# Optimization experiments

Hardware: AMD Instinct MI355X
Metric: run time of the kernel (lower is better)

The kernel has to match this reference:

```python
import jax, jax.numpy as jnp
import numpy as np
from jax import lax

B, T, L, HID = 128, 8, 8, 64  # batch, horizon(=num_layers), lstm layers, hidden

def setup_inputs() -> dict:
    key = jax.random.key(0)
    ks = jax.random.split(key, 40)
    def rn(i, shape, s=0.02):
        return jax.random.normal(ks[i], shape, dtype=jnp.float32) * s
    inp = {
        'image_data': jax.random.normal(ks[0], (B, 3, 192, 256), jnp.float32),
        'action_input_data': jax.random.normal(ks[1], (B, T, 2), jnp.float32),
        'ground_truth_data': jax.random.normal(ks[2], (B, T, 6), jnp.float32),
        'conv1_w': rn(3, (32, 3, 5, 5)), 'conv1_b': rn(4, (32,)),
        'conv2_w': rn(5, (64, 32, 3, 3)), 'conv2_b': rn(6, (64,)),
        'conv3_w': rn(7, (64, 64, 3, 3)), 'conv3_b': rn(8, (64,)),
        'fc1_w': rn(9, (256, 42240)), 'fc1_b': rn(10, (256,)),
        'fc2_w': rn(11, (128, 256)), 'fc2_b': rn(12, (128,)),
        'lowd1_w': rn(13, (128, 128)), 'lowd1_b': rn(14, (128,)),
        'lowd2_w': rn(15, (128, 128)), 'lowd2_b': rn(16, (128,)),
        'act1_w': rn(17, (16, 2)), 'act1_b': rn(18, (16,)),
        'act2_w': rn(19, (16, 16)), 'act2_b': rn(20, (16,)),
        'lstm_Wih0': rn(21, (4 * HID, 16)),
        'lstm_Wih': rn(22, (L - 1, 4 * HID, HID)),
        'lstm_Whh': rn(23, (L, 4 * HID, HID)),
        'lstm_bih': rn(24, (L, 4 * HID)),
        'lstm_bhh': rn(25, (L, 4 * HID)),
        'out1_w': rn(26, (32, 64)), 'out1_b': rn(27, (32,)),
        'out2_w': rn(28, (4, 32)), 'out2_b': rn(29, (4,)),
        'BATCH_SIZE': B, 'horizon': T,
    }
    return inp

def _lin(x, w, b):
    return x @ w.T + b

def _conv(x, w, b):
    y = lax.conv_general_dilated(x, w, (2, 2), 'VALID',
                                 dimension_numbers=('NCHW', 'OIHW', 'NCHW'))
    return y + b[None, :, None, None]

def _lstm(x, h0, c0, Wih0, Wih, Whh, bih, bhh):
    # x: (B,T,16); h0/c0: (L,B,HID). PyTorch gate order: i,f,g,o.
    inp = x
    for l in range(L):
        Wih_l = Wih0 if l == 0 else Wih[l - 1]
        bih_l, bhh_l, Whh_l = bih[l], bhh[l], Whh[l]
        def step(carry, xt):
            h, c = carry
            g = xt @ Wih_l.T + bih_l + h @ Whh_l.T + bhh_l
            i_, f_, g_, o_ = jnp.split(g, 4, axis=-1)
            c = jax.nn.sigmoid(f_) * c + jax.nn.sigmoid(i_) * jnp.tanh(g_)
            h = jax.nn.sigmoid(o_) * jnp.tanh(c)
            return (h, c), h
        _, ys = lax.scan(step, (h0[l], c0[l]), jnp.swapaxes(inp, 0, 1))
        inp = jnp.swapaxes(ys, 0, 1)  # (B,T,HID)
    return inp

def reference(image_data, action_input_data, ground_truth_data,
              conv1_w, conv1_b, conv2_w, conv2_b, conv3_w, conv3_b,
              fc1_w, fc1_b, fc2_w, fc2_b,
              lowd1_w, lowd1_b, lowd2_w, lowd2_b,
              act1_w, act1_b, act2_w, act2_b,
              lstm_Wih0, lstm_Wih, lstm_Whh, lstm_bih, lstm_bhh,
              out1_w, out1_b, out2_w, out2_b,
              BATCH_SIZE, horizon):
    # CNN image pipeline
    x = jax.nn.relu(_conv(image_data, conv1_w, conv1_b))
    x = jax.nn.relu(_conv(x, conv2_w, conv2_b))
    x = _conv(x, conv3_w, conv3_b)
    x = x.reshape(x.shape[0], -1)  # (B, 42240)
    x = jax.nn.relu(_lin(x, fc1_w, fc1_b))
    cnn_out1 = _lin(x, fc2_w, fc2_b)  # (B,128)
    cnn_out2 = _lin(jax.nn.relu(_lin(cnn_out1, lowd1_w, lowd1_b)), lowd2_w, lowd2_b)
    # action pipeline
    a = _lin(jax.nn.relu(_lin(action_input_data, act1_w, act1_b)), act2_w, act2_b)
    # split: first 64 -> c0, second 64 -> h0; broadcast over layers
    c_tmp, h_tmp = cnn_out2[:, :HID], cnn_out2[:, HID:]
    h0 = jnp.broadcast_to(h_tmp[None], (L, h_tmp.shape[0], HID))
    c0 = jnp.broadcast_to(c_tmp[None], (L, c_tmp.shape[0], HID))
    lstm_out = _lstm(a, h0, c0, lstm_Wih0, lstm_Wih, lstm_Whh, lstm_bih, lstm_bhh)
    mo = _lin(jax.nn.relu(_lin(lstm_out, out1_w, out1_b)), out2_w, out2_b)  # (B,T,4)
    # batched yaw rotation (vectorizes the original per-sample loop)
    yaw = ground_truth_data[:, 0, 5]
    cy, sy = jnp.cos(yaw), jnp.sin(yaw)
    z, o = jnp.zeros_like(cy), jnp.ones_like(cy)
    rot = jnp.stack([cy, -sy, z, sy, cy, z, z, z, o], axis=-1).reshape(-1, 3, 3)
    pos = jnp.einsum('bti,bij->btj', mo[:, :, :3], rot) + ground_truth_data[:, 0, 1:4][:, None, :]
    return jnp.concatenate([pos, mo[:, :, 3:4]], axis=-1)
```

## Files before the change

kernel.cpp:

```cpp
#include <hip/hip_runtime.h>
#include <cstdint>

#define DEV __device__ __forceinline__

typedef __attribute__((ext_vector_type(8))) short bf16x8;
typedef __attribute__((ext_vector_type(4))) float f32x4;
typedef __attribute__((ext_vector_type(2))) __fp16 h2t;
typedef __attribute__((ext_vector_type(4))) unsigned int u32x4;
typedef unsigned long long u64;

DEV unsigned short f2bf(float f) {
    unsigned u = __float_as_uint(f);
    unsigned r = u + 0x7fffu + ((u >> 16) & 1u);
    return (unsigned short)(r >> 16);
}
DEV uint32_t pkbf2(float a, float b) {
    return (uint32_t)f2bf(a) | ((uint32_t)f2bf(b) << 16);
}
DEV uint32_t pkh2(float a, float b) {
    h2t p = __builtin_amdgcn_cvt_pkrtz(a, b);
    union { h2t h; uint32_t u; } c;
    c.h = p;
    return c.u;
}
DEV float dot2(uint32_t w, uint32_t x, float acc) {
    union { uint32_t u; h2t h; } a, b;
    a.u = w; b.u = x;
    return __builtin_amdgcn_fdot2(a.h, b.h, acc, false);
}
DEV float sigm(float x) { return __builtin_amdgcn_rcpf(1.f + __expf(-x)); }
DEV float tanh_(float x) { return fmaf(2.f, sigm(2.f * x), -1.f); }
DEV uint32_t packpair(float h) {
    float hs = __int_as_float(__builtin_amdgcn_ds_swizzle(__float_as_int(h), 0x041F));
    return pkh2(h, hs);
}
DEV uint32_t comp4v(u32x4 v, int e) {
    return (e == 0) ? v[0] : (e == 1) ? v[1] : (e == 2) ? v[2] : v[3];
}
DEV u64 pack4bf(float a, float b, float c, float d) {
    unsigned lo = (unsigned)f2bf(a) | ((unsigned)f2bf(b) << 16);
    unsigned hi = (unsigned)f2bf(c) | ((unsigned)f2bf(d) << 16);
    return (u64)lo | ((u64)hi << 32);
}

__global__ __launch_bounds__(256) void k_wprep(const float* __restrict__ w1,
                                               const float* __restrict__ w2,
                                               const float* __restrict__ w3,
                                               unsigned short* __restrict__ w1t,
                                               unsigned short* __restrict__ w2t,
                                               unsigned short* __restrict__ w3t) {
    int i = blockIdx.x * 256 + threadIdx.x;
    if (i < 32 * 128) {
        int oc = i >> 7, k = i & 127;
        int cc = k >> 3, u = (k >> 2) & 1, c = k & 3;
        int r = cc / 3, kx = 2 * (cc - 3 * r) + u;
        w1t[i] = (cc < 15 && kx < 5 && c < 3) ? f2bf(w1[oc * 75 + c * 25 + r * 5 + kx])
                                              : (unsigned short)0;
    } else if (i < 32 * 128 + 64 * 288) {
        int j = i - 32 * 128;
        int oc = j / 288, k = j - oc * 288;
        int pos = k >> 5, c = k & 31;
        int ocr = ((c >> 2) & 1) * 16 + (c >> 3) * 4 + (c & 3);
        w2t[j] = f2bf(w2[oc * 288 + ocr * 9 + pos]);
    } else if (i < 32 * 128 + 64 * 288 + 64 * 576) {
        int j = i - 32 * 128 - 64 * 288;
        int oc = j / 576, k = j - oc * 576;
        int pos = k >> 6, c = k & 63;
        w3t[j] = f2bf(w3[oc * 576 + c * 9 + pos]);
    }
}

__global__ __launch_bounds__(256) void k_wprep_lstm(const float* __restrict__ Wih0,
                                                    const float* __restrict__ Wih,
                                                    const float* __restrict__ Whh,
                                                    uint32_t* __restrict__ wpk) {
    int idx = blockIdx.x * 256 + threadIdx.x;
    int lane = idx & 63;
    int j = (idx >> 6) & 63;
    int l = idx >> 12;
    int g = j >> 4, q = j & 15;
    int r = g * 64 + lane;
    uint32_t ov[4];
#pragma unroll
    for (int e = 0; e < 4; ++e) {
        int p = q * 4 + e;
        float w0, w1;
        if (p < 32) {
            int k0 = 2 * p;
            if (l == 0) {
                w0 = (k0 < 16) ? Wih0[r * 16 + k0] : 0.f;
                w1 = (k0 + 1 < 16) ? Wih0[r * 16 + k0 + 1] : 0.f;
            } else {
                const float* base = Wih + ((size_t)(l - 1) * 256 + r) * 64;
                w0 = base[k0];
                w1 = base[k0 + 1];
            }
        } else {
            int k0 = 2 * (p - 32);
            const float* base = Whh + ((size_t)l * 256 + r) * 64;
            w0 = base[k0];
            w1 = base[k0 + 1];
        }
        ov[e] = pkh2(w0, w1);
    }
    uint4 v;
    v.x = ov[0]; v.y = ov[1]; v.z = ov[2]; v.w = ov[3];
    ((uint4*)wpk)[idx] = v;
}

__global__ __launch_bounds__(256, 3) void k_conv1m(const float* __restrict__ img,
                                                   const unsigned short* __restrict__ w1t,
                                                   const float* __restrict__ bias,
                                                   unsigned short* __restrict__ out) {
    int b = blockIdx.x, y0 = blockIdx.y * 4;
    int tid = threadIdx.x;
    __shared__ __align__(16) unsigned short lds[12 * 1040];
    char* lb = (char*)lds;
    const float* ib = img + (size_t)b * 3 * 192 * 256;
    float t0[11], t1[11], t2[11];
#pragma unroll
    for (int r = 0; r < 11; ++r) {
        int row = 2 * y0 + r;
        if (row > 191) row = 191;
        const float* ip = ib + row * 256 + tid;
        t0[r] = ip[0];
        t1[r] = ip[192 * 256];
        t2[r] = ip[2 * 192 * 256];
    }
    __builtin_amdgcn_sched_barrier(0);
#pragma unroll
    for (int r = 0; r < 11; ++r) {
        uint32_t lo = (uint32_t)f2bf(t0[r]) | ((uint32_t)f2bf(t1[r]) << 16);
        *(u64*)(lb + r * 2080 + tid * 8) = (u64)lo | ((u64)f2bf(t2[r]) << 32);
    }
    *(u64*)(lb + 11 * 2080 + tid * 8) = 0ull;
    __syncthreads();
    int wave = tid >> 6, lane = tid & 63;
    int quad = lane >> 4, nl = lane & 15;
    int ly = wave;
    float4 bv0 = *(const float4*)(bias + quad * 4);
    float4 bv1 = *(const float4*)(bias + 16 + quad * 4);
    f32x4 acc[8][2];
#pragma unroll
    for (int nt = 0; nt < 8; ++nt) {
        acc[nt][0][0] = bv0.x; acc[nt][0][1] = bv0.y; acc[nt][0][2] = bv0.z; acc[nt][0][3] = bv0.w;
        acc[nt][1][0] = bv1.x; acc[nt][1][1] = bv1.y; acc[nt][1][2] = bv1.z; acc[nt][1][3] = bv1.w;
    }
#pragma unroll
    for (int ks = 0; ks < 4; ++ks) {
        int cc = ks * 4 + quad;
        int r = cc / 3, kxp = cc - 3 * r;
        int rb = (2 * ly + r) * 2080 + kxp * 16 + nl * 16;
        bf16x8 af0 = *(const bf16x8*)(w1t + (nl) * 128 + ks * 32 + quad * 8);
        bf16x8 af1 = *(const bf16x8*)(w1t + (16 + nl) * 128 + ks * 32 + quad * 8);
#pragma unroll
        for (int nt = 0; nt < 8; ++nt) {
            bf16x8 bv = *(const bf16x8*)(lb + rb + nt * 256);
            acc[nt][0] = __builtin_amdgcn_mfma_f32_16x16x32_bf16(af0, bv, acc[nt][0], 0, 0, 0);
            acc[nt][1] = __builtin_amdgcn_mfma_f32_16x16x32_bf16(af1, bv, acc[nt][1], 0, 0, 0);
        }
    }
    int y = y0 + ly;
    if (y < 94) {
#pragma unroll
        for (int nt = 0; nt < 8; ++nt) {
            int x = nt * 16 + nl;
            if (x < 126) {
                f32x4 a0 = acc[nt][0], a1 = acc[nt][1];
                u64 lo = pack4bf(fmaxf(a0[0], 0.f), fmaxf(a0[1], 0.f),
                                 fmaxf(a0[2], 0.f), fmaxf(a0[3], 0.f));
                u64 hi = pack4bf(fmaxf(a1[0], 0.f), fmaxf(a1[1], 0.f),
                                 fmaxf(a1[2], 0.f), fmaxf(a1[3], 0.f));
                uint4 st;
                st.x = (uint32_t)lo; st.y = (uint32_t)(lo >> 32);
                st.z = (uint32_t)hi; st.w = (uint32_t)(hi >> 32);
                *(uint4*)(out + (((size_t)b * 94 + y) * 126 + x) * 32 + quad * 8) = st;
            }
        }
    }
}

__global__ __launch_bounds__(256, 1) void k_conv2m(const unsigned short* __restrict__ in,
                                                   const unsigned short* __restrict__ w2t,
                                                   const float* __restrict__ bias,
                                                   unsigned short* __restrict__ out) {
    int b = blockIdx.x, xh = blockIdx.y, yh = blockIdx.z;
    int tid = threadIdx.x;
    int wave = tid >> 6, lane = tid & 63;
    int quad = lane >> 4, nl = lane & 15;
    int mtg = wave & 1, ntg = wave >> 1;
    __shared__ __align__(16) char lds[4 * 4680];
    const u64* in64 = (const u64*)in;

    bf16x8 wfa[9], wfb[9];
#pragma unroll
    for (int ks = 0; ks < 9; ++ks) {
        wfa[ks] = *(const bf16x8*)(w2t + ((mtg * 2 + 0) * 16 + nl) * 288 + ks * 32 + quad * 8);
        wfb[ks] = *(const bf16x8*)(w2t + ((mtg * 2 + 1) * 16 + nl) * 288 + ks * 32 + quad * 8);
    }
    float4 bv0 = *(const float4*)(bias + (mtg * 2 + 0) * 16 + quad * 4);
    float4 bv1 = *(const float4*)(bias + (mtg * 2 + 1) * 16 + quad * 4);

    int y0 = yh * 23;
    int rr = tid >> 7, li = tid & 127;

    {
        int y2 = 2 * y0 + rr;
        const u64* s = in64 + ((size_t)(b * 94 + y2) * 126 + 62 * xh) * 8;
        int slot = y2 & 3;
        u64 g0[4];
#pragma unroll
        for (int j = 0; j < 4; ++j) { int idx = li + j * 128; g0[j] = (idx < 504) ? s[idx] : 0ull; }
#pragma unroll
        for (int j = 0; j < 4; ++j) {
            int idx = li + j * 128;
            if (idx < 504) *(u64*)(lds + slot * 4680 + (idx >> 3) * 72 + (idx & 7) * 8) = g0[j];
        }
        int y2b = 2 * y0 + 2;
        const u64* s2 = in64 + ((size_t)(b * 94 + y2b) * 126 + 62 * xh) * 8;
        int slot2 = y2b & 3;
        u64 g1[2];
#pragma unroll
        for (int j = 0; j < 2; ++j) { int idx = tid + j * 256; g1[j] = (idx < 504) ? s2[idx] : 0ull; }
#pragma unroll
        for (int j = 0; j < 2; ++j) {
            int idx = tid + j * 256;
            if (idx < 504) *(u64*)(lds + slot2 * 4680 + (idx >> 3) * 72 + (idx & 7) * 8) = g1[j];
        }
    }
    u64 g[4];
    {
        int y2 = 2 * y0 + 3 + rr;
        const u64* s = in64 + ((size_t)(b * 94 + y2) * 126 + 62 * xh) * 8;
#pragma unroll
        for (int j = 0; j < 4; ++j) { int idx = li + j * 128; g[j] = (idx < 504) ? s[idx] : 0ull; }
    }
    __syncthreads();

    int xl = ntg * 16 + nl;
    for (int yy = 0; yy < 23; ++yy) {
        int y = y0 + yy;
        f32x4 acc0, acc1;
        acc0[0] = bv0.x; acc0[1] = bv0.y; acc0[2] = bv0.z; acc0[3] = bv0.w;
        acc1[0] = bv1.x; acc1[1] = bv1.y; acc1[2] = bv1.z; acc1[3] = bv1.w;
        int sb0 = ((2 * y) & 3) * 4680;
        int sb1 = ((2 * y + 1) & 3) * 4680;
        int sb2 = ((2 * y + 2) & 3) * 4680;
#pragma unroll
        for (int ks = 0; ks < 9; ++ks) {
            const int r = ks / 3, kx = ks - r * 3;
            int sb = (r == 0) ? sb0 : (r == 1) ? sb1 : sb2;
            union { u64 d[2]; bf16x8 v; } bb;
            const char* base = lds + sb + (2 * xl + kx) * 72 + quad * 16;
            bb.d[0] = *(const u64*)(base);
            bb.d[1] = *(const u64*)(base + 8);
            acc0 = __builtin_amdgcn_mfma_f32_16x16x32_bf16(wfa[ks], bb.v, acc0, 0, 0, 0);
            acc1 = __builtin_amdgcn_mfma_f32_16x16x32_bf16(wfb[ks], bb.v, acc1, 0, 0, 0);
        }
        if (xl < 31) {
            int xg = xh * 31 + xl;
            u64 p0 = pack4bf(fmaxf(acc0[0], 0.f), fmaxf(acc0[1], 0.f),
                             fmaxf(acc0[2], 0.f), fmaxf(acc0[3], 0.f));
            u64 p1 = pack4bf(fmaxf(acc1[0], 0.f), fmaxf(acc1[1], 0.f),
                             fmaxf(acc1[2], 0.f), fmaxf(acc1[3], 0.f));
            *(u64*)(out + (((size_t)b * 46 + y) * 62 + xg) * 64 + (mtg * 2 + 0) * 16 + quad * 4) = p0;
            *(u64*)(out + (((size_t)b * 46 + y) * 62 + xg) * 64 + (mtg * 2 + 1) * 16 + quad * 4) = p1;
        }
        __syncthreads();
        {
            int row = 2 * y + 3 + rr;
            int slot = row & 3;
#pragma unroll
            for (int j = 0; j < 4; ++j) {
                int idx = li + j * 128;
                if (idx < 504) *(u64*)(lds + slot * 4680 + (idx >> 3) * 72 + (idx & 7) * 8) = g[j];
            }
        }
        if (yy < 22) {
            int y2 = 2 * y + 5 + rr;
            if (y2 > 93) y2 = 93;
            const u64* s = in64 + ((size_t)(b * 94 + y2) * 126 + 62 * xh) * 8;
#pragma unroll
            for (int j = 0; j < 4; ++j) { int idx = li + j * 128; g[j] = (idx < 504) ? s[idx] : 0ull; }
        }
        __syncthreads();
    }
}

__global__ __launch_bounds__(256, 1) void k_conv3m(const unsigned short* __restrict__ in,
                                                   const unsigned short* __restrict__ w3t,
                                                   const float* __restrict__ bias,
                                                   unsigned short* __restrict__ out) {
    int b = blockIdx.x, xh = blockIdx.y, yh = blockIdx.z;
    int tid = threadIdx.x;
    int wave = tid >> 6, lane = tid & 63;
    int quad = lane >> 4, nl = lane & 15;
    __shared__ __align__(16) char lds[4 * 4488];
    const u64* in64 = (const u64*)in;

    bf16x8 wf[18];
#pragma unroll
    for (int ks = 0; ks < 18; ++ks)
        wf[ks] = *(const bf16x8*)(w3t + (wave * 16 + nl) * 576 + ks * 32 + quad * 8);
    float4 bv = *(const float4*)(bias + wave * 16 + quad * 4);

    int y0 = yh * 11;
    int rr = tid >> 7, li = tid & 127;

    {
        int y2 = 2 * y0 + rr;
        const u64* s = in64 + ((size_t)(b * 46 + y2) * 62 + 30 * xh) * 16;
        int slot = y2 & 3;
        u64 g0[4];
#pragma unroll
        for (int j = 0; j < 4; ++j) { int idx = li + j * 128; g0[j] = (idx < 496) ? s[idx] : 0ull; }
#pragma unroll
        for (int j = 0; j < 4; ++j) {
            int idx = li + j * 128;
            if (idx < 496) *(u64*)(lds + slot * 4488 + (idx >> 4) * 136 + (idx & 15) * 8) = g0[j];
        }
        int y2b = 2 * y0 + 2;
        const u64* s2 = in64 + ((size_t)(b * 46 + y2b) * 62 + 30 * xh) * 16;
        int slot2 = y2b & 3;
        u64 g1[2];
#pragma unroll
        for (int j = 0; j < 2; ++j) { int idx = tid + j * 256; g1[j] = (idx < 496) ? s2[idx] : 0ull; }
#pragma unroll
        for (int j = 0; j < 2; ++j) {
            int idx = tid + j * 256;
            if (idx < 496) *(u64*)(lds + slot2 * 4488 + (idx >> 4) * 136 + (idx & 15) * 8) = g1[j];
        }
    }
    u64 g[4];
    {
        int y2 = 2 * y0 + 3 + rr;
        const u64* s = in64 + ((size_t)(b * 46 + y2) * 62 + 30 * xh) * 16;
#pragma unroll
        for (int j = 0; j < 4; ++j) { int idx = li + j * 128; g[j] = (idx < 496) ? s[idx] : 0ull; }
    }
    __syncthreads();

    for (int yy = 0; yy < 11; ++yy) {
        int y = y0 + yy;
        f32x4 acc;
        acc[0] = bv.x; acc[1] = bv.y; acc[2] = bv.z; acc[3] = bv.w;
        int sb0 = ((2 * y) & 3) * 4488;
        int sb1 = ((2 * y + 1) & 3) * 4488;
        int sb2 = ((2 * y + 2) & 3) * 4488;
#pragma unroll
        for (int ks = 0; ks < 18; ++ks) {
            const int pos = ks >> 1, half = ks & 1;
            const int r = pos / 3, kx = pos - r * 3;
            int sb = (r == 0) ? sb0 : (r == 1) ? sb1 : sb2;
            union { u64 d[2]; bf16x8 v; } bb;
            const char* base = lds + sb + (2 * nl + kx) * 136 + half * 64 + quad * 16;
            bb.d[0] = *(const u64*)(base);
            bb.d[1] = *(const u64*)(base + 8);
            acc = __builtin_amdgcn_mfma_f32_16x16x32_bf16(wf[ks], bb.v, acc, 0, 0, 0);
        }
        if (nl < 15) {
            int xg = xh * 15 + nl;
#pragma unroll
            for (int r2 = 0; r2 < 4; ++r2)
                out[(size_t)b * 42240 + (wave * 16 + quad * 4 + r2) * 660 + y * 30 + xg] = f2bf(acc[r2]);
        }
        __syncthreads();
        {
            int row = 2 * y + 3 + rr;
            int slot = row & 3;
#pragma unroll
            for (int j = 0; j < 4; ++j) {
                int idx = li + j * 128;
                if (idx < 496) *(u64*)(lds + slot * 4488 + (idx >> 4) * 136 + (idx & 15) * 8) = g[j];
            }
        }
        if (yy < 10) {
            int y2 = 2 * y + 5 + rr;
            if (y2 > 45) y2 = 45;
            const u64* s = in64 + ((size_t)(b * 46 + y2) * 62 + 30 * xh) * 16;
#pragma unroll
            for (int j = 0; j < 4; ++j) { int idx = li + j * 128; g[j] = (idx < 496) ? s[idx] : 0ull; }
        }
        __syncthreads();
    }
}

__global__ __launch_bounds__(256) void k_fc1_mfma(const unsigned short* __restrict__ A,
                                                  const float* __restrict__ W,
                                                  float* __restrict__ part) {
    int kc = blockIdx.x;
    int nb = blockIdx.y;
    int tid = threadIdx.x;
    int wave = tid >> 6, lane = tid & 63;
    int m16 = lane & 15, quad = lane >> 4;
    __shared__ __align__(16) char lw[2][64 * 80];
    __shared__ __align__(16) char la[2][128 * 80];
    int k0 = kc * 704;
    int wrow = tid >> 2, wseg = tid & 3;
    const float* wsrc = W + (size_t)(nb * 64 + wrow) * 42240 + k0 + wseg * 8;
    int arow = tid >> 1, aseg = tid & 1;
    const uint4* asrc = (const uint4*)(A + (size_t)arow * 42240 + k0) + aseg * 2;
    float4 wr0 = ((const float4*)wsrc)[0];
    float4 wr1 = ((const float4*)wsrc)[1];
    uint4 ar0 = asrc[0];
    uint4 ar1 = asrc[1];
    f32x4 acc[8] = {};
    for (int ks = 0; ks < 22; ++ks) {
        int buf = ks & 1;
        uint4 wp;
        wp.x = pkbf2(wr0.x, wr0.y); wp.y = pkbf2(wr0.z, wr0.w);
        wp.z = pkbf2(wr1.x, wr1.y); wp.w = pkbf2(wr1.z, wr1.w);
        *(uint4*)(lw[buf] + wrow * 80 + wseg * 16) = wp;
        *(uint4*)(la[buf] + arow * 80 + aseg * 32) = ar0;
        *(uint4*)(la[buf] + arow * 80 + aseg * 32 + 16) = ar1;
        if (ks < 21) {
            wsrc += 32;
            asrc += 4;
            wr0 = ((const float4*)wsrc)[0];
            wr1 = ((const float4*)wsrc)[1];
            ar0 = asrc[0];
            ar1 = asrc[1];
        }
        __syncthreads();
        bf16x8 wf = *(const bf16x8*)(lw[buf] + (wave * 16 + m16) * 80 + quad * 16);
        const char* lab = la[buf] + m16 * 80 + quad * 16;
#pragma unroll
        for (int tm = 0; tm < 8; ++tm) {
            bf16x8 af = *(const bf16x8*)(lab + tm * 16 * 80);
            acc[tm] = __builtin_amdgcn_mfma_f32_16x16x32_bf16(af, wf, acc[tm], 0, 0, 0);
        }
    }
    int n = nb * 64 + wave * 16 + m16;
    float* pb = part + ((size_t)kc * 128) * 256 + n;
#pragma unroll
    for (int tm = 0; tm < 8; ++tm) {
        int row = tm * 16 + quad * 4;
#pragma unroll
        for (int r = 0; r < 4; ++r) pb[(size_t)(row + r) * 256] = acc[tm][r];
    }
}

__global__ __launch_bounds__(256) void k_head(const float* __restrict__ part,
                                              const float* __restrict__ f1b,
                                              const float* __restrict__ w2, const float* __restrict__ b2,
                                              const float* __restrict__ lw1, const float* __restrict__ lb1,
                                              const float* __restrict__ lw2, const float* __restrict__ lb2,
                                              float* __restrict__ cnn2) {
    int b = blockIdx.x, t = threadIdx.x;
    __shared__ float xa[256];
    __shared__ float xb[128];
    __shared__ float xc[128];
    __shared__ float pp[256];
    float s = f1b[t];
#pragma unroll
    for (int kc = 0; kc < 60; ++kc) s += part[((size_t)kc * 128 + b) * 256 + t];
    xa[t] = fmaxf(s, 0.f);
    __syncthreads();
    int n = t & 127, half = t >> 7;
    float acc = half ? 0.f : b2[n];
    {
        const float* w2r = w2 + n * 256 + half * 128;
        const float* xar = xa + half * 128;
#pragma unroll
        for (int k = 0; k < 128; ++k) acc = fmaf(xar[k], w2r[k], acc);
    }
    pp[t] = acc;
    __syncthreads();
    if (t < 128) xb[t] = pp[t] + pp[t + 128];
    __syncthreads();
    acc = half ? 0.f : lb1[n];
    {
        const float* l1r = lw1 + n * 128 + half * 64;
        const float* xbr = xb + half * 64;
#pragma unroll
        for (int k = 0; k < 64; ++k) acc = fmaf(xbr[k], l1r[k], acc);
    }
    pp[t] = acc;
    __syncthreads();
    if (t < 128) xc[t] = fmaxf(pp[t] + pp[t + 128], 0.f);
    __syncthreads();
    acc = half ? 0.f : lb2[n];
    {
        const float* l2r = lw2 + n * 128 + half * 64;
        const float* xcr = xc + half * 64;
#pragma unroll
        for (int k = 0; k < 64; ++k) acc = fmaf(xcr[k], l2r[k], acc);
    }
    pp[t] = acc;
    __syncthreads();
    if (t < 128) cnn2[b * 128 + t] = pp[t] + pp[t + 128];
}

__global__ __launch_bounds__(256) void k_act(const float* __restrict__ ain,
                                             const float* __restrict__ w1, const float* __restrict__ b1,
                                             const float* __restrict__ w2, const float* __restrict__ b2,
                                             float* __restrict__ abuf) {
    int idx = blockIdx.x * 256 + threadIdx.x;
    float x0 = ain[idx * 2], x1 = ain[idx * 2 + 1];
    float h1[16];
#pragma unroll
    for (int i = 0; i < 16; ++i)
        h1[i] = fmaxf(fmaf(x0, w1[i * 2], fmaf(x1, w1[i * 2 + 1], b1[i])), 0.f);
#pragma unroll
    for (int i = 0; i < 16; ++i) {
        float a = b2[i];
#pragma unroll
        for (int j = 0; j < 16; ++j) a = fmaf(h1[j], w2[i * 16 + j], a);
        abuf[idx * 16 + i] = a;
    }
}

__global__ __launch_bounds__(512, 2) void k_lstm(const float* __restrict__ abuf,
                                                 const float* __restrict__ cnn2,
                                                 const uint32_t* __restrict__ wpk,
                                                 const float* __restrict__ bih,
                                                 const float* __restrict__ bhh,
                                                 float* __restrict__ lout) {
    int b = blockIdx.x;
    int tid = threadIdx.x;
    int w = tid >> 6, lane = tid & 63;
    int sl = w >> 1, pt = w & 1;
    __shared__ uint32_t hbuf[2][3][32];
    __shared__ uint32_t h3pk[8][32];
    __shared__ float4 pex[8][64];

    uint32_t xq[8];
#pragma unroll
    for (int t = 0; t < 8; ++t) {
        float x0 = 0.f, x1 = 0.f;
        if (lane < 8) {
            const float* ap = abuf + (b * 8 + t) * 16 + 2 * lane;
            x0 = ap[0];
            x1 = ap[1];
        }
        xq[t] = pkh2(x0, x1);
    }
    float h0 = cnn2[b * 128 + 64 + lane];
    float c0 = cnn2[b * 128 + lane];
    const u32x4* wbase = (const u32x4*)wpk;

#pragma unroll
    for (int P = 0; P < 2; ++P) {
        const int L = P * 4 + sl;
        u32x4 wreg[4][8];
#pragma unroll
        for (int g = 0; g < 4; ++g)
#pragma unroll
            for (int q = 0; q < 8; ++q)
                wreg[g][q] = wbase[(size_t)L * 4096 + (g * 16 + pt * 8 + q) * 64 + lane];
        float bias0 = 0.f, bias1 = 0.f, bias2 = 0.f, bias3 = 0.f;
        if (pt == 0) {
            bias0 = bih[L * 256 + lane] + bhh[L * 256 + lane];
            bias1 = bih[L * 256 + 64 + lane] + bhh[L * 256 + 64 + lane];
            bias2 = bih[L * 256 + 128 + lane] + bhh[L * 256 + 128 + lane];
            bias3 = bih[L * 256 + 192 + lane] + bhh[L * 256 + 192 + lane];
        }
        float h = h0, c = c0;
        uint32_t hpk = packpair(h0);

        for (int s = 0; s < 11; ++s) {
            bool act = (s >= sl && s < sl + 8);
            float a0 = bias0, a1 = bias1, a2 = bias2, a3 = bias3;
            if (act) {
                if (pt == 0) {
                    uint32_t xcur;
                    if (sl == 0)
                        xcur = (P == 0) ? xq[0] : h3pk[s][lane & 31];
                    else
                        xcur = hbuf[(s & 1) ^ 1][sl - 1][lane & 31];
#pragma unroll
                    for (int m = 0; m < 32; ++m) {
                        uint32_t bx = (uint32_t)__builtin_amdgcn_readlane((int)xcur, m);
                        int q = m >> 2, e = m & 3;
                        a0 = dot2(comp4v(wreg[0][q], e), bx, a0);
                        a1 = dot2(comp4v(wreg[1][q], e), bx, a1);
                        a2 = dot2(comp4v(wreg[2][q], e), bx, a2);
                        a3 = dot2(comp4v(wreg[3][q], e), bx, a3);
                    }
                } else {
#pragma unroll
                    for (int m = 0; m < 32; ++m) {
                        uint32_t bh2 = (uint32_t)__builtin_amdgcn_readlane((int)hpk, 2 * m);
                        int q = m >> 2, e = m & 3;
                        a0 = dot2(comp4v(wreg[0][q], e), bh2, a0);
                        a1 = dot2(comp4v(wreg[1][q], e), bh2, a1);
                        a2 = dot2(comp4v(wreg[2][q], e), bh2, a2);
                        a3 = dot2(comp4v(wreg[3][q], e), bh2, a3);
                    }
                }
                float4 pv;
                pv.x = a0; pv.y = a1; pv.z = a2; pv.w = a3;
                pex[w][lane] = pv;
            }
            __syncthreads();
            if (act) {
                float4 po = pex[w ^ 1][lane];
                float g0 = a0 + po.x, g1 = a1 + po.y, g2 = a2 + po.z, g3 = a3 + po.w;
                float gi = sigm(g0), gf = sigm(g1), gv = tanh_(g2), go = sigm(g3);
                c = gf * c + gi * gv;
                h = go * tanh_(c);
                hpk = packpair(h);
                if (pt == 0) {
                    if (sl < 3) {
                        if (!(lane & 1)) hbuf[s & 1][sl][lane >> 1] = hpk;
                    } else if (P == 0) {
                        if (!(lane & 1)) h3pk[s - 3][lane >> 1] = hpk;
                    } else {
                        lout[((size_t)b * 8 + (s - 3)) * 64 + lane] = h;
                    }
                }
            }
            if (P == 0 && w == 0) {
#pragma unroll
                for (int k = 0; k < 7; ++k) xq[k] = xq[k + 1];
            }
            __syncthreads();
        }
    }
}

__global__ __launch_bounds__(256) void k_out(const float* __restrict__ lout,
                                             const float* __restrict__ w1, const float* __restrict__ b1,
                                             const float* __restrict__ w2, const float* __restrict__ b2,
                                             const float* __restrict__ gt, float* __restrict__ out) {
    int idx = blockIdx.x * 256 + threadIdx.x;
    int b = idx >> 3;
    float x[64];
#pragma unroll
    for (int j = 0; j < 64; ++j) x[j] = lout[idx * 64 + j];
    float h[32];
#pragma unroll 8
    for (int i = 0; i < 32; ++i) {
        float a = b1[i];
#pragma unroll
        for (int j = 0; j < 64; ++j) a = fmaf(x[j], w1[i * 64 + j], a);
        h[i] = fmaxf(a, 0.f);
    }
    float mo[4];
#pragma unroll
    for (int i = 0; i < 4; ++i) {
        float a = b2[i];
#pragma unroll
        for (int j = 0; j < 32; ++j) a = fmaf(h[j], w2[i * 32 + j], a);
        mo[i] = a;
    }
    float yaw = gt[b * 48 + 5];
    float cy = cosf(yaw), sy = sinf(yaw);
    out[idx * 4 + 0] = fmaf(mo[0], cy, fmaf(mo[1], sy, gt[b * 48 + 1]));
    out[idx * 4 + 1] = fmaf(mo[0], -sy, fmaf(mo[1], cy, gt[b * 48 + 2]));
    out[idx * 4 + 2] = mo[2] + gt[b * 48 + 3];
    out[idx * 4 + 3] = mo[3];
}

extern "C" void kernel_launch(void* const* d_in, const int* in_sizes, int n_in,
                              void* d_out, int out_size, void* d_ws, size_t ws_size,
                              hipStream_t stream) {
    const float* img = (const float*)d_in[0];
    const float* ain = (const float*)d_in[1];
    const float* gt = (const float*)d_in[2];
    const float* c1w = (const float*)d_in[3];
    const float* c1b = (const float*)d_in[4];
    const float* c2w = (const float*)d_in[5];
    const float* c2b = (const float*)d_in[6];
    const float* c3w = (const float*)d_in[7];
    const float* c3b = (const float*)d_in[8];
    const float* f1w = (const float*)d_in[9];
    const float* f1b = (const float*)d_in[10];
    const float* f2w = (const float*)d_in[11];
    const float* f2b = (const float*)d_in[12];
    const float* l1w = (const float*)d_in[13];
    const float* l1b = (const float*)d_in[14];
    const float* l2w = (const float*)d_in[15];
    const float* l2b = (const float*)d_in[16];
    const float* a1w = (const float*)d_in[17];
    const float* a1b = (const float*)d_in[18];
    const float* a2w = (const float*)d_in[19];
    const float* a2b = (const float*)d_in[20];
    const float* wih0 = (const float*)d_in[21];
    const float* wih = (const float*)d_in[22];
    const float* whh = (const float*)d_in[23];
    const float* bihp = (const float*)d_in[24];
    const float* bhhp = (const float*)d_in[25];
    const float* o1w = (const float*)d_in[26];
    const float* o1b = (const float*)d_in[27];
    const float* o2w = (const float*)d_in[28];
    const float* o2b = (const float*)d_in[29];
    float* out = (float*)d_out;

    char* ws = (char*)d_ws;
    unsigned short* c1o = (unsigned short*)(ws);
    unsigned short* c2o = (unsigned short*)(ws + 97026048);
    unsigned short* c3o = (unsigned short*)(ws + 143753216);
    float* f1p = (float*)(ws + 154566656);
    float* cnn2 = (float*)(ws + 163348480);
    float* abuf = (float*)(ws + 163414016);
    float* lo = (float*)(ws + 163479552);
    unsigned short* w1t = (unsigned short*)(ws + 163741696);
    unsigned short* w2t = (unsigned short*)(ws + 163749888);
    unsigned short* w3t = (unsigned short*)(ws + 163786752);
    uint32_t* wpk = (uint32_t*)(ws + 163860480);

    k_wprep<<<232, 256, 0, stream>>>(c1w, c2w, c3w, w1t, w2t, w3t);
    k_wprep_lstm<<<128, 256, 0, stream>>>(wih0, wih, whh, wpk);
    k_conv1m<<<dim3(128, 24), 256, 0, stream>>>(img, w1t, c1b, c1o);
    k_conv2m<<<dim3(128, 2, 2), 256, 0, stream>>>(c1o, w2t, c2b, c2o);
    k_conv3m<<<dim3(128, 2, 2), 256, 0, stream>>>(c2o, w3t, c3b, c3o);
    k_fc1_mfma<<<dim3(60, 4), 256, 0, stream>>>(c3o, f1w, f1p);
    k_head<<<128, 256, 0, stream>>>(f1p, f1b, f2w, f2b, l1w, l1b, l2w, l2b, cnn2);
    k_act<<<4, 256, 0, stream>>>(ain, a1w, a1b, a2w, a2b, abuf);
    k_lstm<<<128, 512, 0, stream>>>(abuf, cnn2, wpk, bihp, bhhp, lo);
    k_out<<<4, 256, 0, stream>>>(lo, o1w, o1b, o2w, o2b, gt, out);
}
```

Before: 357.3 us.

## Loop conv1 blocks over output rows with ring-buffered LDS and prefetched input rows

Each conv1 block now produces 24 output rows in six iterations instead of 4 rows, so the grid drops from 24 to 4 blocks per image. The 16-slot LDS ring reuses the overlapping input rows between iterations. The next 8 input rows are prefetched into registers while the current MFMAs run, and weight fragments are hoisted out of the loop. This cuts redundant halo loads and per-block setup, at the cost of fewer blocks (512 total), a lower occupancy hint, and extra barriers per iteration.

```diff
diff --git a/kernel.cpp b/kernel.cpp
--- a/kernel.cpp
+++ b/kernel.cpp
@@ -108,74 +108,119 @@
     ((uint4*)wpk)[idx] = v;
 }
 
-__global__ __launch_bounds__(256, 3) void k_conv1m(const float* __restrict__ img,
+__global__ __launch_bounds__(256, 2) void k_conv1m(const float* __restrict__ img,
                                                    const unsigned short* __restrict__ w1t,
                                                    const float* __restrict__ bias,
                                                    unsigned short* __restrict__ out) {
-    int b = blockIdx.x, y0 = blockIdx.y * 4;
+    int b = blockIdx.x, yh = blockIdx.y;
+    int y0 = yh * 24;
     int tid = threadIdx.x;
-    __shared__ __align__(16) unsigned short lds[12 * 1040];
+    __shared__ __align__(16) unsigned short lds[16 * 1040];
     char* lb = (char*)lds;
     const float* ib = img + (size_t)b * 3 * 192 * 256;
-    float t0[11], t1[11], t2[11];
-#pragma unroll
-    for (int r = 0; r < 11; ++r) {
-        int row = 2 * y0 + r;
+    int R0 = 2 * y0;
+
+    int wave = tid >> 6, lane = tid & 63;
+    int quad = lane >> 4, nl = lane & 15;
+    bf16x8 af0[4], af1[4];
+#pragma unroll
+    for (int ks = 0; ks < 4; ++ks) {
+        af0[ks] = *(const bf16x8*)(w1t + nl * 128 + ks * 32 + quad * 8);
+        af1[ks] = *(const bf16x8*)(w1t + (16 + nl) * 128 + ks * 32 + quad * 8);
+    }
+    float4 bv0 = *(const float4*)(bias + quad * 4);
+    float4 bv1 = *(const float4*)(bias + 16 + quad * 4);
+
+    {
+        float t0[11], t1[11], t2[11];
+#pragma unroll
+        for (int r = 0; r < 11; ++r) {
+            int row = R0 + r;
+            if (row > 191) row = 191;
+            const float* ip = ib + row * 256 + tid;
+            t0[r] = ip[0];
+            t1[r] = ip[192 * 256];
+            t2[r] = ip[2 * 192 * 256];
+        }
+        __builtin_amdgcn_sched_barrier(0);
+#pragma unroll
+        for (int r = 0; r < 11; ++r) {
+            uint32_t lo = (uint32_t)f2bf(t0[r]) | ((uint32_t)f2bf(t1[r]) << 16);
+            *(u64*)(lb + r * 2080 + tid * 8) = (u64)lo | ((u64)f2bf(t2[r]) << 32);
+        }
+        *(u64*)(lb + 11 * 2080 + tid * 8) = 0ull;
+    }
+    float g0[8], g1[8], g2[8];
+#pragma unroll
+    for (int r = 0; r < 8; ++r) {
+        int row = R0 + 11 + r;
         if (row > 191) row = 191;
         const float* ip = ib + row * 256 + tid;
-        t0[r] = ip[0];
-        t1[r] = ip[192 * 256];
-        t2[r] = ip[2 * 192 * 256];
-    }
-    __builtin_amdgcn_sched_barrier(0);
-#pragma unroll
-    for (int r = 0; r < 11; ++r) {
-        uint32_t lo = (uint32_t)f2bf(t0[r]) | ((uint32_t)f2bf(t1[r]) << 16);
-        *(u64*)(lb + r * 2080 + tid * 8) = (u64)lo | ((u64)f2bf(t2[r]) << 32);
-    }
-    *(u64*)(lb + 11 * 2080 + tid * 8) = 0ull;
-    __syncthreads();
-    int wave = tid >> 6, lane = tid & 63;
-    int quad = lane >> 4, nl = lane & 15;
-    int ly = wave;
-    float4 bv0 = *(const float4*)(bias + quad * 4);
-    float4 bv1 = *(const float4*)(bias + 16 + quad * 4);
-    f32x4 acc[8][2];
-#pragma unroll
-    for (int nt = 0; nt < 8; ++nt) {
-        acc[nt][0][0] = bv0.x; acc[nt][0][1] = bv0.y; acc[nt][0][2] = bv0.z; acc[nt][0][3] = bv0.w;
-        acc[nt][1][0] = bv1.x; acc[nt][1][1] = bv1.y; acc[nt][1][2] = bv1.z; acc[nt][1][3] = bv1.w;
-    }
-#pragma unroll
-    for (int ks = 0; ks < 4; ++ks) {
-        int cc = ks * 4 + quad;
-        int r = cc / 3, kxp = cc - 3 * r;
-        int rb = (2 * ly + r) * 2080 + kxp * 16 + nl * 16;
-        bf16x8 af0 = *(const bf16x8*)(w1t + (nl) * 128 + ks * 32 + quad * 8);
-        bf16x8 af1 = *(const bf16x8*)(w1t + (16 + nl) * 128 + ks * 32 + quad * 8);
+        g0[r] = ip[0];
+        g1[r] = ip[192 * 256];
+        g2[r] = ip[2 * 192 * 256];
+    }
+    __syncthreads();
+
+    for (int it = 0; it < 6; ++it) {
+        int R = R0 + 8 * it;
+        int y = y0 + it * 4 + wave;
+        f32x4 acc[8][2];
 #pragma unroll
         for (int nt = 0; nt < 8; ++nt) {
-            bf16x8 bv = *(const bf16x8*)(lb + rb + nt * 256);
-            acc[nt][0] = __builtin_amdgcn_mfma_f32_16x16x32_bf16(af0, bv, acc[nt][0], 0, 0, 0);
-            acc[nt][1] = __builtin_amdgcn_mfma_f32_16x16x32_bf16(af1, bv, acc[nt][1], 0, 0, 0);
-        }
-    }
-    int y = y0 + ly;
-    if (y < 94) {
-#pragma unroll
-        for (int nt = 0; nt < 8; ++nt) {
-            int x = nt * 16 + nl;
-            if (x < 126) {
-                f32x4 a0 = acc[nt][0], a1 = acc[nt][1];
-                u64 lo = pack4bf(fmaxf(a0[0], 0.f), fmaxf(a0[1], 0.f),
-                                 fmaxf(a0[2], 0.f), fmaxf(a0[3], 0.f));
-                u64 hi = pack4bf(fmaxf(a1[0], 0.f), fmaxf(a1[1], 0.f),
-                                 fmaxf(a1[2], 0.f), fmaxf(a1[3], 0.f));
-                uint4 st;
-                st.x = (uint32_t)lo; st.y = (uint32_t)(lo >> 32);
-                st.z = (uint32_t)hi; st.w = (uint32_t)(hi >> 32);
-                *(uint4*)(out + (((size_t)b * 94 + y) * 126 + x) * 32 + quad * 8) = st;
-            }
+            acc[nt][0][0] = bv0.x; acc[nt][0][1] = bv0.y; acc[nt][0][2] = bv0.z; acc[nt][0][3] = bv0.w;
+            acc[nt][1][0] = bv1.x; acc[nt][1][1] = bv1.y; acc[nt][1][2] = bv1.z; acc[nt][1][3] = bv1.w;
+        }
+#pragma unroll
+        for (int ks = 0; ks < 4; ++ks) {
+            int cc = ks * 4 + quad;
+            int r = cc / 3, kxp = cc - 3 * r;
+            int slot = (R + 2 * wave + r) & 15;
+            int rb = slot * 2080 + kxp * 16 + nl * 16;
+#pragma unroll
+            for (int nt = 0; nt < 8; ++nt) {
+                bf16x8 bv = *(const bf16x8*)(lb + rb + nt * 256);
+                acc[nt][0] = __builtin_amdgcn_mfma_f32_16x16x32_bf16(af0[ks], bv, acc[nt][0], 0, 0, 0);
+                acc[nt][1] = __builtin_amdgcn_mfma_f32_16x16x32_bf16(af1[ks], bv, acc[nt][1], 0, 0, 0);
+            }
+        }
+        if (y < 94) {
+#pragma unroll
+            for (int nt = 0; nt < 8; ++nt) {
+                int x = nt * 16 + nl;
+                if (x < 126) {
+                    f32x4 a0 = acc[nt][0], a1 = acc[nt][1];
+                    u64 lo = pack4bf(fmaxf(a0[0], 0.f), fmaxf(a0[1], 0.f),
+                                     fmaxf(a0[2], 0.f), fmaxf(a0[3], 0.f));
+                    u64 hi = pack4bf(fmaxf(a1[0], 0.f), fmaxf(a1[1], 0.f),
+                                     fmaxf(a1[2], 0.f), fmaxf(a1[3], 0.f));
+                    uint4 st;
+                    st.x = (uint32_t)lo; st.y = (uint32_t)(lo >> 32);
+                    st.z = (uint32_t)hi; st.w = (uint32_t)(hi >> 32);
+                    *(uint4*)(out + (((size_t)b * 94 + y) * 126 + x) * 32 + quad * 8) = st;
+                }
+            }
+        }
+        if (it < 5) {
+            __syncthreads();
+#pragma unroll
+            for (int r = 0; r < 8; ++r) {
+                int slot = (R + 11 + r) & 15;
+                uint32_t lo = (uint32_t)f2bf(g0[r]) | ((uint32_t)f2bf(g1[r]) << 16);
+                *(u64*)(lb + slot * 2080 + tid * 8) = (u64)lo | ((u64)f2bf(g2[r]) << 32);
+            }
+            if (it < 4) {
+#pragma unroll
+                for (int r = 0; r < 8; ++r) {
+                    int row = R + 19 + r;
+                    if (row > 191) row = 191;
+                    const float* ip = ib + row * 256 + tid;
+                    g0[r] = ip[0];
+                    g1[r] = ip[192 * 256];
+                    g2[r] = ip[2 * 192 * 256];
+                }
+            }
+            __syncthreads();
         }
     }
 }
@@ -702,7 +747,7 @@
 
     k_wprep<<<232, 256, 0, stream>>>(c1w, c2w, c3w, w1t, w2t, w3t);
     k_wprep_lstm<<<128, 256, 0, stream>>>(wih0, wih, whh, wpk);
-    k_conv1m<<<dim3(128, 24), 256, 0, stream>>>(img, w1t, c1b, c1o);
+    k_conv1m<<<dim3(128, 4), 256, 0, stream>>>(img, w1t, c1b, c1o);
     k_conv2m<<<dim3(128, 2, 2), 256, 0, stream>>>(c1o, w2t, c2b, c2o);
     k_conv3m<<<dim3(128, 2, 2), 256, 0, stream>>>(c2o, w3t, c3b, c3o);
     k_fc1_mfma<<<dim3(60, 4), 256, 0, stream>>>(c3o, f1w, f1p);
```

Measured after the change: 348.0 us. -2.6%, faster.

## Fuse conv1 into conv2 with rolling LDS row buffers

Applied to the files above, without the earlier changes.

Merges the conv1 and conv2 kernels into one. Each block now stages image rows in a rolling LDS ring, computes conv1 output rows on the fly into a second LDS ring, and consumes them directly for conv2. This removes the ~97MB bf16 conv1 intermediate write and read through global memory, plus one launch. In exchange, conv1 halo rows are recomputed at the x/y tile borders, there are more barriers per row, and only 512 blocks run with one block per CU, which lowers occupancy.

```diff
diff --git a/kernel.cpp b/kernel.cpp
--- a/kernel.cpp
+++ b/kernel.cpp
@@ -108,180 +108,156 @@
     ((uint4*)wpk)[idx] = v;
 }
 
-__global__ __launch_bounds__(256, 3) void k_conv1m(const float* __restrict__ img,
+__global__ __launch_bounds__(256, 1) void k_conv12(const float* __restrict__ img,
                                                    const unsigned short* __restrict__ w1t,
-                                                   const float* __restrict__ bias,
-                                                   unsigned short* __restrict__ out) {
-    int b = blockIdx.x, y0 = blockIdx.y * 4;
-    int tid = threadIdx.x;
-    __shared__ __align__(16) unsigned short lds[12 * 1040];
-    char* lb = (char*)lds;
-    const float* ib = img + (size_t)b * 3 * 192 * 256;
-    float t0[11], t1[11], t2[11];
-#pragma unroll
-    for (int r = 0; r < 11; ++r) {
-        int row = 2 * y0 + r;
-        if (row > 191) row = 191;
-        const float* ip = ib + row * 256 + tid;
-        t0[r] = ip[0];
-        t1[r] = ip[192 * 256];
-        t2[r] = ip[2 * 192 * 256];
-    }
-    __builtin_amdgcn_sched_barrier(0);
-#pragma unroll
-    for (int r = 0; r < 11; ++r) {
-        uint32_t lo = (uint32_t)f2bf(t0[r]) | ((uint32_t)f2bf(t1[r]) << 16);
-        *(u64*)(lb + r * 2080 + tid * 8) = (u64)lo | ((u64)f2bf(t2[r]) << 32);
-    }
-    *(u64*)(lb + 11 * 2080 + tid * 8) = 0ull;
-    __syncthreads();
-    int wave = tid >> 6, lane = tid & 63;
-    int quad = lane >> 4, nl = lane & 15;
-    int ly = wave;
-    float4 bv0 = *(const float4*)(bias + quad * 4);
-    float4 bv1 = *(const float4*)(bias + 16 + quad * 4);
-    f32x4 acc[8][2];
-#pragma unroll
-    for (int nt = 0; nt < 8; ++nt) {
-        acc[nt][0][0] = bv0.x; acc[nt][0][1] = bv0.y; acc[nt][0][2] = bv0.z; acc[nt][0][3] = bv0.w;
-        acc[nt][1][0] = bv1.x; acc[nt][1][1] = bv1.y; acc[nt][1][2] = bv1.z; acc[nt][1][3] = bv1.w;
-    }
-#pragma unroll
-    for (int ks = 0; ks < 4; ++ks) {
-        int cc = ks * 4 + quad;
-        int r = cc / 3, kxp = cc - 3 * r;
-        int rb = (2 * ly + r) * 2080 + kxp * 16 + nl * 16;
-        bf16x8 af0 = *(const bf16x8*)(w1t + (nl) * 128 + ks * 32 + quad * 8);
-        bf16x8 af1 = *(const bf16x8*)(w1t + (16 + nl) * 128 + ks * 32 + quad * 8);
-#pragma unroll
-        for (int nt = 0; nt < 8; ++nt) {
-            bf16x8 bv = *(const bf16x8*)(lb + rb + nt * 256);
-            acc[nt][0] = __builtin_amdgcn_mfma_f32_16x16x32_bf16(af0, bv, acc[nt][0], 0, 0, 0);
-            acc[nt][1] = __builtin_amdgcn_mfma_f32_16x16x32_bf16(af1, bv, acc[nt][1], 0, 0, 0);
-        }
-    }
-    int y = y0 + ly;
-    if (y < 94) {
-#pragma unroll
-        for (int nt = 0; nt < 8; ++nt) {
-            int x = nt * 16 + nl;
-            if (x < 126) {
-                f32x4 a0 = acc[nt][0], a1 = acc[nt][1];
-                u64 lo = pack4bf(fmaxf(a0[0], 0.f), fmaxf(a0[1], 0.f),
-                                 fmaxf(a0[2], 0.f), fmaxf(a0[3], 0.f));
-                u64 hi = pack4bf(fmaxf(a1[0], 0.f), fmaxf(a1[1], 0.f),
-                                 fmaxf(a1[2], 0.f), fmaxf(a1[3], 0.f));
-                uint4 st;
-                st.x = (uint32_t)lo; st.y = (uint32_t)(lo >> 32);
-                st.z = (uint32_t)hi; st.w = (uint32_t)(hi >> 32);
-                *(uint4*)(out + (((size_t)b * 94 + y) * 126 + x) * 32 + quad * 8) = st;
-            }
-        }
-    }
-}
-
-__global__ __launch_bounds__(256, 1) void k_conv2m(const unsigned short* __restrict__ in,
+                                                   const float* __restrict__ b1,
                                                    const unsigned short* __restrict__ w2t,
-                                                   const float* __restrict__ bias,
+                                                   const float* __restrict__ b2,
                                                    unsigned short* __restrict__ out) {
     int b = blockIdx.x, xh = blockIdx.y, yh = blockIdx.z;
     int tid = threadIdx.x;
-    int wave = tid >> 6, lane = tid & 63;
+    int w = tid >> 6, lane = tid & 63;
     int quad = lane >> 4, nl = lane & 15;
-    int mtg = wave & 1, ntg = wave >> 1;
-    __shared__ __align__(16) char lds[4 * 4680];
-    const u64* in64 = (const u64*)in;
-
-    bf16x8 wfa[9], wfb[9];
+    int nh = w >> 1, rw = w & 1;
+    __shared__ __align__(16) char ldsI[8 * 2080];
+    __shared__ __align__(16) char ldsC[4 * 4536];
+    const float* ib = img + (size_t)b * 3 * 192 * 256;
+    int y0 = yh * 23;
+    int imx = 124 * xh + tid;
+    bool stg = tid < 132;
+
+    bf16x8 wa1[4], wb1[4];
+#pragma unroll
+    for (int ks = 0; ks < 4; ++ks) {
+        wa1[ks] = *(const bf16x8*)(w1t + nl * 128 + ks * 32 + quad * 8);
+        wb1[ks] = *(const bf16x8*)(w1t + (16 + nl) * 128 + ks * 32 + quad * 8);
+    }
+    bf16x8 wa2[9], wb2[9];
 #pragma unroll
     for (int ks = 0; ks < 9; ++ks) {
-        wfa[ks] = *(const bf16x8*)(w2t + ((mtg * 2 + 0) * 16 + nl) * 288 + ks * 32 + quad * 8);
-        wfb[ks] = *(const bf16x8*)(w2t + ((mtg * 2 + 1) * 16 + nl) * 288 + ks * 32 + quad * 8);
-    }
-    float4 bv0 = *(const float4*)(bias + (mtg * 2 + 0) * 16 + quad * 4);
-    float4 bv1 = *(const float4*)(bias + (mtg * 2 + 1) * 16 + quad * 4);
-
-    int y0 = yh * 23;
-    int rr = tid >> 7, li = tid & 127;
+        wa2[ks] = *(const bf16x8*)(w2t + ((rw * 2 + 0) * 16 + nl) * 288 + ks * 32 + quad * 8);
+        wb2[ks] = *(const bf16x8*)(w2t + ((rw * 2 + 1) * 16 + nl) * 288 + ks * 32 + quad * 8);
+    }
+    float4 c1b0 = *(const float4*)(b1 + quad * 4);
+    float4 c1b1 = *(const float4*)(b1 + 16 + quad * 4);
+    float4 c2b0 = *(const float4*)(b2 + (rw * 2 + 0) * 16 + quad * 4);
+    float4 c2b1 = *(const float4*)(b2 + (rw * 2 + 1) * 16 + quad * 4);
+
+    auto ldimg = [&](int row, float& f0, float& f1, float& f2) {
+        if (row > 191) row = 191;
+        const float* ip = ib + row * 256 + imx;
+        f0 = ip[0];
+        f1 = ip[192 * 256];
+        f2 = ip[2 * 192 * 256];
+    };
+    auto stimg = [&](int row, float f0, float f1, float f2) {
+        uint32_t lo = (uint32_t)f2bf(f0) | ((uint32_t)f2bf(f1) << 16);
+        *(u64*)(ldsI + (row & 7) * 2080 + imx * 8) = (u64)lo | ((u64)f2bf(f2) << 32);
+    };
+    auto conv1row = [&](int R1) {
+        f32x4 a00, a01;
+        a00[0] = c1b0.x; a00[1] = c1b0.y; a00[2] = c1b0.z; a00[3] = c1b0.w;
+        a01[0] = c1b1.x; a01[1] = c1b1.y; a01[2] = c1b1.z; a01[3] = c1b1.w;
+        f32x4 a10 = a00, a11 = a01;
+#pragma unroll
+        for (int ks = 0; ks < 4; ++ks) {
+            int cc = ks * 4 + quad;
+            int r = cc / 3, kxp = cc - 3 * r;
+            int rb = ((2 * R1 + r) & 7) * 2080 + 992 * xh + 512 * nh + kxp * 16 + nl * 16;
+            bf16x8 v0 = *(const bf16x8*)(ldsI + rb);
+            bf16x8 v1 = *(const bf16x8*)(ldsI + rb + 256);
+            a00 = __builtin_amdgcn_mfma_f32_16x16x32_bf16(wa1[ks], v0, a00, 0, 0, 0);
+            a01 = __builtin_amdgcn_mfma_f32_16x16x32_bf16(wb1[ks], v0, a01, 0, 0, 0);
+            a10 = __builtin_amdgcn_mfma_f32_16x16x32_bf16(wa1[ks], v1, a10, 0, 0, 0);
+            a11 = __builtin_amdgcn_mfma_f32_16x16x32_bf16(wb1[ks], v1, a11, 0, 0, 0);
+        }
+        int cs = (R1 & 3) * 4536;
+        int xl0 = nh * 32 + nl;
+        {
+            u64 lo = pack4bf(fmaxf(a00[0], 0.f), fmaxf(a00[1], 0.f),
+                             fmaxf(a00[2], 0.f), fmaxf(a00[3], 0.f));
+            u64 hi = pack4bf(fmaxf(a01[0], 0.f), fmaxf(a01[1], 0.f),
+                             fmaxf(a01[2], 0.f), fmaxf(a01[3], 0.f));
+            uint4 st;
+            st.x = (uint32_t)lo; st.y = (uint32_t)(lo >> 32);
+            st.z = (uint32_t)hi; st.w = (uint32_t)(hi >> 32);
+            *(uint4*)(ldsC + cs + xl0 * 72 + quad * 16) = st;
+        }
+        int xl1 = xl0 + 16;
+        if (xl1 < 63) {
+            u64 lo = pack4bf(fmaxf(a10[0], 0.f), fmaxf(a10[1], 0.f),
+                             fmaxf(a10[2], 0.f), fmaxf(a10[3], 0.f));
+            u64 hi = pack4bf(fmaxf(a11[0], 0.f), fmaxf(a11[1], 0.f),
+                             fmaxf(a11[2], 0.f), fmaxf(a11[3], 0.f));
+            uint4 st;
+            st.x = (uint32_t)lo; st.y = (uint32_t)(lo >> 32);
+            st.z = (uint32_t)hi; st.w = (uint32_t)(hi >> 32);
+            *(uint4*)(ldsC + cs + xl1 * 72 + quad * 16) = st;
+        }
+    };
 
     {
-        int y2 = 2 * y0 + rr;
-        const u64* s = in64 + ((size_t)(b * 94 + y2) * 126 + 62 * xh) * 8;
-        int slot = y2 & 3;
-        u64 g0[4];
-#pragma unroll
-        for (int j = 0; j < 4; ++j) { int idx = li + j * 128; g0[j] = (idx < 504) ? s[idx] : 0ull; }
-#pragma unroll
-        for (int j = 0; j < 4; ++j) {
-            int idx = li + j * 128;
-            if (idx < 504) *(u64*)(lds + slot * 4680 + (idx >> 3) * 72 + (idx & 7) * 8) = g0[j];
-        }
-        int y2b = 2 * y0 + 2;
-        const u64* s2 = in64 + ((size_t)(b * 94 + y2b) * 126 + 62 * xh) * 8;
-        int slot2 = y2b & 3;
-        u64 g1[2];
-#pragma unroll
-        for (int j = 0; j < 2; ++j) { int idx = tid + j * 256; g1[j] = (idx < 504) ? s2[idx] : 0ull; }
-#pragma unroll
-        for (int j = 0; j < 2; ++j) {
-            int idx = tid + j * 256;
-            if (idx < 504) *(u64*)(lds + slot2 * 4680 + (idx >> 3) * 72 + (idx & 7) * 8) = g1[j];
-        }
-    }
-    u64 g[4];
-    {
-        int y2 = 2 * y0 + 3 + rr;
-        const u64* s = in64 + ((size_t)(b * 94 + y2) * 126 + 62 * xh) * 8;
-#pragma unroll
-        for (int j = 0; j < 4; ++j) { int idx = li + j * 128; g[j] = (idx < 504) ? s[idx] : 0ull; }
-    }
-    __syncthreads();
-
-    int xl = ntg * 16 + nl;
-    for (int yy = 0; yy < 23; ++yy) {
-        int y = y0 + yy;
-        f32x4 acc0, acc1;
-        acc0[0] = bv0.x; acc0[1] = bv0.y; acc0[2] = bv0.z; acc0[3] = bv0.w;
-        acc1[0] = bv1.x; acc1[1] = bv1.y; acc1[2] = bv1.z; acc1[3] = bv1.w;
-        int sb0 = ((2 * y) & 3) * 4680;
-        int sb1 = ((2 * y + 1) & 3) * 4680;
-        int sb2 = ((2 * y + 2) & 3) * 4680;
-#pragma unroll
-        for (int ks = 0; ks < 9; ++ks) {
-            const int r = ks / 3, kx = ks - r * 3;
-            int sb = (r == 0) ? sb0 : (r == 1) ? sb1 : sb2;
-            union { u64 d[2]; bf16x8 v; } bb;
-            const char* base = lds + sb + (2 * xl + kx) * 72 + quad * 16;
-            bb.d[0] = *(const u64*)(base);
-            bb.d[1] = *(const u64*)(base + 8);
-            acc0 = __builtin_amdgcn_mfma_f32_16x16x32_bf16(wfa[ks], bb.v, acc0, 0, 0, 0);
-            acc1 = __builtin_amdgcn_mfma_f32_16x16x32_bf16(wfb[ks], bb.v, acc1, 0, 0, 0);
-        }
-        if (xl < 31) {
-            int xg = xh * 31 + xl;
-            u64 p0 = pack4bf(fmaxf(acc0[0], 0.f), fmaxf(acc0[1], 0.f),
-                             fmaxf(acc0[2], 0.f), fmaxf(acc0[3], 0.f));
-            u64 p1 = pack4bf(fmaxf(acc1[0], 0.f), fmaxf(acc1[1], 0.f),
-                             fmaxf(acc1[2], 0.f), fmaxf(acc1[3], 0.f));
-            *(u64*)(out + (((size_t)b * 46 + y) * 62 + xg) * 64 + (mtg * 2 + 0) * 16 + quad * 4) = p0;
-            *(u64*)(out + (((size_t)b * 46 + y) * 62 + xg) * 64 + (mtg * 2 + 1) * 16 + quad * 4) = p1;
+        float p0[8], p1[8], p2[8];
+        if (stg) {
+#pragma unroll
+            for (int r = 0; r < 8; ++r) ldimg(4 * y0 + r, p0[r], p1[r], p2[r]);
+        }
+        __builtin_amdgcn_sched_barrier(0);
+        if (stg) {
+#pragma unroll
+            for (int r = 0; r < 8; ++r) stimg(4 * y0 + r, p0[r], p1[r], p2[r]);
+        }
+    }
+    __syncthreads();
+    conv1row(2 * y0 + rw);
+    float g0[4], g1[4], g2[4];
+    if (stg) {
+#pragma unroll
+        for (int r = 0; r < 4; ++r) ldimg(4 * y0 + 8 + r, g0[r], g1[r], g2[r]);
+    }
+    __syncthreads();
+    if (stg) {
+#pragma unroll
+        for (int r = 0; r < 4; ++r) stimg(4 * y0 + 8 + r, g0[r], g1[r], g2[r]);
+    }
+    __syncthreads();
+
+    for (int t = 0; t < 23; ++t) {
+        int y = y0 + t;
+        conv1row(2 * y + 2 + rw);
+        if (stg) {
+#pragma unroll
+            for (int r = 0; r < 4; ++r) ldimg(4 * y + 12 + r, g0[r], g1[r], g2[r]);
         }
         __syncthreads();
         {
-            int row = 2 * y + 3 + rr;
-            int slot = row & 3;
-#pragma unroll
-            for (int j = 0; j < 4; ++j) {
-                int idx = li + j * 128;
-                if (idx < 504) *(u64*)(lds + slot * 4680 + (idx >> 3) * 72 + (idx & 7) * 8) = g[j];
+            f32x4 acc0, acc1;
+            acc0[0] = c2b0.x; acc0[1] = c2b0.y; acc0[2] = c2b0.z; acc0[3] = c2b0.w;
+            acc1[0] = c2b1.x; acc1[1] = c2b1.y; acc1[2] = c2b1.z; acc1[3] = c2b1.w;
+            int xl = nh * 16 + nl;
+#pragma unroll
+            for (int ks = 0; ks < 9; ++ks) {
+                int r = ks / 3, kx = ks - r * 3;
+                const char* base = ldsC + ((2 * y + r) & 3) * 4536 + (2 * xl + kx) * 72 + quad * 16;
+                union { u64 d[2]; bf16x8 v; } bb;
+                bb.d[0] = *(const u64*)(base);
+                bb.d[1] = *(const u64*)(base + 8);
+                acc0 = __builtin_amdgcn_mfma_f32_16x16x32_bf16(wa2[ks], bb.v, acc0, 0, 0, 0);
+                acc1 = __builtin_amdgcn_mfma_f32_16x16x32_bf16(wb2[ks], bb.v, acc1, 0, 0, 0);
             }
-        }
-        if (yy < 22) {
-            int y2 = 2 * y + 5 + rr;
-            if (y2 > 93) y2 = 93;
-            const u64* s = in64 + ((size_t)(b * 94 + y2) * 126 + 62 * xh) * 8;
-#pragma unroll
-            for (int j = 0; j < 4; ++j) { int idx = li + j * 128; g[j] = (idx < 504) ? s[idx] : 0ull; }
+            if (xl < 31) {
+                int xg = xh * 31 + xl;
+                u64 q0 = pack4bf(fmaxf(acc0[0], 0.f), fmaxf(acc0[1], 0.f),
+                                 fmaxf(acc0[2], 0.f), fmaxf(acc0[3], 0.f));
+                u64 q1 = pack4bf(fmaxf(acc1[0], 0.f), fmaxf(acc1[1], 0.f),
+                                 fmaxf(acc1[2], 0.f), fmaxf(acc1[3], 0.f));
+                *(u64*)(out + (((size_t)b * 46 + y) * 62 + xg) * 64 + (rw * 2 + 0) * 16 + quad * 4) = q0;
+                *(u64*)(out + (((size_t)b * 46 + y) * 62 + xg) * 64 + (rw * 2 + 1) * 16 + quad * 4) = q1;
+            }
+        }
+        if (stg) {
+#pragma unroll
+            for (int r = 0; r < 4; ++r) stimg(4 * y + 12 + r, g0[r], g1[r], g2[r]);
         }
         __syncthreads();
     }
@@ -688,7 +664,6 @@
     float* out = (float*)d_out;
 
     char* ws = (char*)d_ws;
-    unsigned short* c1o = (unsigned short*)(ws);
     unsigned short* c2o = (unsigned short*)(ws + 97026048);
     unsigned short* c3o = (unsigned short*)(ws + 143753216);
     float* f1p = (float*)(ws + 154566656);
@@ -702,8 +677,7 @@
 
     k_wprep<<<232, 256, 0, stream>>>(c1w, c2w, c3w, w1t, w2t, w3t);
     k_wprep_lstm<<<128, 256, 0, stream>>>(wih0, wih, whh, wpk);
-    k_conv1m<<<dim3(128, 24), 256, 0, stream>>>(img, w1t, c1b, c1o);
-    k_conv2m<<<dim3(128, 2, 2), 256, 0, stream>>>(c1o, w2t, c2b, c2o);
+    k_conv12<<<dim3(128, 2, 2), 256, 0, stream>>>(img, w1t, c1b, w2t, c2b, c2o);
     k_conv3m<<<dim3(128, 2, 2), 256, 0, stream>>>(c2o, w3t, c3b, c3o);
     k_fc1_mfma<<<dim3(60, 4), 256, 0, stream>>>(c3o, f1w, f1p);
     k_head<<<128, 256, 0, stream>>>(f1p, f1b, f2w, f2b, l1w, l1b, l2w, l2b, cnn2);
```

New measurement: 331.8 us. 7.2% less time.
